# Optimization experiments

Measured on AMD Instinct MI355X. Metric: run time of the kernel, lower is better.

## Reference

```python
import jax, jax.numpy as jnp
import numpy as np

B = 8          # batches
NSX = 8        # subdomains per axis
NSY = 8
NSUB = NSX * NSY
GRID = 64      # points per axis per batch -> 64 points per subdomain
N = B * GRID * GRID
HID = 32       # hidden_channels (also v channels)
OUT = 32       # out_channels
TRES = 64      # max points per subdomain (exact here: uniform grid)


def _point_proj(coords, w1, b1, w2, b2, out_ch, in_ch):
    # PointProjection: Linear(2,hid) -> GELU(exact) -> Linear(hid, out*in) -> [P,out,in]
    h = jax.nn.gelu(coords @ w1 + b1, approximate=False)
    k = h @ w2 + b2
    return k.reshape(coords.shape[0], out_ch, in_ch)


def setup_inputs() -> dict:
    key = jax.random.key(0)
    ks = jax.random.split(key, 9)
    # uniform cell-centered point grid per batch in [0,1]^2
    lin = (jnp.arange(GRID, dtype=jnp.float32) + 0.5) / GRID
    X, Y = jnp.meshgrid(lin, lin, indexing='xy')
    coords1 = jnp.stack([X, Y], axis=-1).reshape(-1, 2)
    src_coords = jnp.tile(coords1, (B, 1))                       # [N,2]
    src_batch = jnp.repeat(jnp.arange(B, dtype=jnp.int32), GRID * GRID)
    v = jax.random.normal(ks[0], (N, HID), jnp.float32)

    def lin_w(k, fan_in, shape):
        bound = 1.0 / np.sqrt(fan_in)
        return jax.random.uniform(k, shape, jnp.float32, -bound, bound)

    return {
        'v': v,
        'src_coords': src_coords,
        'src_batch': src_batch,
        'tgt_res': TRES,
        'src_w1': lin_w(ks[1], 2, (2, HID)),
        'src_b1': lin_w(ks[2], 2, (HID,)),
        'src_w2': lin_w(ks[3], HID, (HID, OUT * HID)),
        'src_b2': lin_w(ks[4], HID, (OUT * HID,)),
        'tgt_w1': lin_w(ks[5], 2, (2, HID)),
        'tgt_b1': lin_w(ks[6], 2, (HID,)),
        'tgt_w2': lin_w(ks[7], HID, (HID, OUT * HID)),
        'tgt_b2': lin_w(ks[8], HID, (OUT * HID,)),
    }


def reference(v, src_coords, src_batch, tgt_res,
              src_w1, src_b1, src_w2, src_b2,
              tgt_w1, tgt_b1, tgt_w2, tgt_b2):
    # --- compute_clusters: assign each point to (batch, subdomain) segment ---
    cx = jnp.clip((src_coords[:, 0] * NSX).astype(jnp.int32), 0, NSX - 1)
    cy = jnp.clip((src_coords[:, 1] * NSY).astype(jnp.int32), 0, NSY - 1)
    seg = src_batch * NSUB + cy * NSX + cx                      # [N]
    S = B * NSUB

    # --- reference target grid in [-1/nsx, 1/nsx] x [-1/nsy, 1/nsy] ---
    x = jnp.linspace(-1.0 / NSX, 1.0 / NSX, tgt_res)
    y = jnp.linspace(-1.0 / NSY, 1.0 / NSY, tgt_res)
    TX, TY = jnp.meshgrid(x, y, indexing='xy')
    tgt_coords = jnp.stack([TX, TY], axis=-1).reshape(-1, 2)    # [T,2], T=tgt_res^2

    # --- per-point MLP kernel projections ---
    psi = _point_proj(src_coords, src_w1, src_b1, src_w2, src_b2, OUT, HID)  # [N,OUT,HID]
    phi = _point_proj(tgt_coords, tgt_w1, tgt_b1, tgt_w2, tgt_b2, OUT, HID)  # [T,OUT,HID]

    # --- segment-wise integral: A[s,o,h] = mean_{x in seg s} psi[x,o,h]*v[x,h] ---
    contrib = psi * v[:, None, :]                                # [N,OUT,HID]
    A = jax.ops.segment_sum(contrib, seg, num_segments=S)        # [S,OUT,HID]
    cnt = jax.ops.segment_sum(jnp.ones((v.shape[0],), v.dtype), seg, num_segments=S)
    A = A / jnp.maximum(cnt, 1.0)[:, None, None]

    # --- contract with target kernel on the reference grid ---
    u = jnp.einsum('toh,soh->sto', phi, A)                       # [S,T,OUT]
    u = u.reshape(B, NSUB, tgt_res, tgt_res, OUT)
    return u
```

## Files before the change

### kernel.cpp

```cpp
#include <hip/hip_runtime.h>
#include <hip/hip_bf16.h>

#define HID   32
#define OUT   32
#define T_TOT 4096
#define S_TOT 512

typedef __attribute__((ext_vector_type(8))) short short8;
typedef __attribute__((ext_vector_type(4))) float f32x4;

__device__ __forceinline__ float gelu_exact(float x) {
    return 0.5f * x * (1.0f + erff(x * 0.70710678118654752440f));
}

__device__ __forceinline__ unsigned int f2bf_u(float x) {
    __hip_bfloat16 h = __float2bfloat16(x);
    unsigned short us = *reinterpret_cast<unsigned short*>(&h);
    return (unsigned int)us;
}

__global__ __launch_bounds__(256) void k_seg_G(
    const float* __restrict__ v, const float* __restrict__ coords,
    const float* __restrict__ sw1, const float* __restrict__ sb1,
    const float* __restrict__ sw2, const float* __restrict__ sb2,
    const float* __restrict__ tw2, const float* __restrict__ tb2,
    const float* __restrict__ tw1, const float* __restrict__ tb1,
    unsigned short* __restrict__ Pbf, float* __restrict__ qout,
    unsigned int* __restrict__ Gbf) {
    const int tid = threadIdx.x;

    if (blockIdx.x >= S_TOT) {
        int t = (blockIdx.x - S_TOT) * 256 + tid;
        int i = t >> 6, j = t & 63;
        const double step = 0.25 / 63.0;
        float x = (float)(-0.125 + (double)j * step);
        float y = (float)(-0.125 + (double)i * step);
        unsigned int pk[16];
#pragma unroll
        for (int c2 = 0; c2 < 16; ++c2) {
            float z0 = fmaf(x, tw1[2 * c2],     fmaf(y, tw1[HID + 2 * c2],     tb1[2 * c2]));
            float z1 = fmaf(x, tw1[2 * c2 + 1], fmaf(y, tw1[HID + 2 * c2 + 1], tb1[2 * c2 + 1]));
            pk[c2] = f2bf_u(gelu_exact(z0)) | (f2bf_u(gelu_exact(z1)) << 16);
        }
        uint4* dst = (uint4*)(Gbf + (size_t)t * 16);
#pragma unroll
        for (int k = 0; k < 4; ++k)
            dst[k] = make_uint4(pk[4 * k], pk[4 * k + 1], pk[4 * k + 2], pk[4 * k + 3]);
        return;
    }

    const int s = blockIdx.x;
    const int b = s >> 6, cy = (s >> 3) & 7, cx = s & 7;

    __shared__ float Hs[64][HID];
    __shared__ float Vs[64][HID];
    __shared__ float Ms[HID][HID];
    __shared__ float Vsum[HID];

    {
        int r = tid >> 2, qq = tid & 3;
        int p = b * 4096 + (cy * 8 + (r >> 3)) * 64 + cx * 8 + (r & 7);
        const f32x4* src = (const f32x4*)(v + (size_t)p * HID + qq * 8);
        f32x4 a0 = src[0], a1 = src[1];
        *(f32x4*)&Vs[r][qq * 8]     = a0;
        *(f32x4*)&Vs[r][qq * 8 + 4] = a1;

        float x = coords[2 * p], y = coords[2 * p + 1];
#pragma unroll
        for (int e = 0; e < 8; ++e) {
            int c = qq * 8 + e;
            float z = fmaf(x, sw1[c], fmaf(y, sw1[HID + c], sb1[c]));
            Hs[r][c] = gelu_exact(z);
        }
    }
    __syncthreads();

    if (tid < 128) {
        int cp = tid >> 3, hq = tid & 7;
        int c0 = cp * 2;
        f32x4 accA = {0.f, 0.f, 0.f, 0.f};
        f32x4 accB = {0.f, 0.f, 0.f, 0.f};
#pragma unroll 16
        for (int r = 0; r < 64; ++r) {
            float2 hv = *(const float2*)&Hs[r][c0];
            f32x4 vv = *(const f32x4*)&Vs[r][hq * 4];
            accA[0] = fmaf(hv.x, vv[0], accA[0]);
            accA[1] = fmaf(hv.x, vv[1], accA[1]);
            accA[2] = fmaf(hv.x, vv[2], accA[2]);
            accA[3] = fmaf(hv.x, vv[3], accA[3]);
            accB[0] = fmaf(hv.y, vv[0], accB[0]);
            accB[1] = fmaf(hv.y, vv[1], accB[1]);
            accB[2] = fmaf(hv.y, vv[2], accB[2]);
            accB[3] = fmaf(hv.y, vv[3], accB[3]);
        }
        *(f32x4*)&Ms[c0][hq * 4]     = accA;
        *(f32x4*)&Ms[c0 + 1][hq * 4] = accB;
    } else if (tid < 160) {
        int h = tid - 128;
        float sum = 0.f;
#pragma unroll 16
        for (int r = 0; r < 64; ++r) sum += Vs[r][h];
        Vsum[h] = sum;
    }
    __syncthreads();

    {
        int o = tid >> 3, hq = tid & 7;
        f32x4 acc = {0.f, 0.f, 0.f, 0.f};
#pragma unroll 8
        for (int c = 0; c < HID; ++c) {
            f32x4 w = *(const f32x4*)(sw2 + (size_t)c * 1024 + o * 32 + hq * 4);
            f32x4 m = *(const f32x4*)&Ms[c][hq * 4];
            acc[0] = fmaf(m[0], w[0], acc[0]);
            acc[1] = fmaf(m[1], w[1], acc[1]);
            acc[2] = fmaf(m[2], w[2], acc[2]);
            acc[3] = fmaf(m[3], w[3], acc[3]);
        }
        f32x4 bb = *(const f32x4*)(sb2 + o * 32 + hq * 4);
        f32x4 vs = *(const f32x4*)&Vsum[hq * 4];
        acc[0] = fmaf(bb[0], vs[0], acc[0]);
        acc[1] = fmaf(bb[1], vs[1], acc[1]);
        acc[2] = fmaf(bb[2], vs[2], acc[2]);
        acc[3] = fmaf(bb[3], vs[3], acc[3]);
        const float inv = 1.0f / 64.0f;
        acc[0] *= inv; acc[1] *= inv; acc[2] *= inv; acc[3] *= inv;

        f32x4 a[8];
        int base = (o & 7) * 8;
#pragma unroll
        for (int k = 0; k < 8; ++k) {
            a[k][0] = __shfl(acc[0], base + k, 64);
            a[k][1] = __shfl(acc[1], base + k, 64);
            a[k][2] = __shfl(acc[2], base + k, 64);
            a[k][3] = __shfl(acc[3], base + k, 64);
        }

        int cq = hq;
        unsigned int pk[2];
#pragma unroll
        for (int k2 = 0; k2 < 2; ++k2) {
            unsigned int w01 = 0;
#pragma unroll
            for (int kk = 0; kk < 2; ++kk) {
                int c = cq * 4 + k2 * 2 + kk;
                float pacc = 0.f;
#pragma unroll
                for (int h8 = 0; h8 < 8; ++h8) {
                    f32x4 w = *(const f32x4*)(tw2 + (size_t)c * 1024 + o * 32 + h8 * 4);
                    pacc = fmaf(w[0], a[h8][0], pacc);
                    pacc = fmaf(w[1], a[h8][1], pacc);
                    pacc = fmaf(w[2], a[h8][2], pacc);
                    pacc = fmaf(w[3], a[h8][3], pacc);
                }
                w01 |= f2bf_u(pacc) << (16 * kk);
            }
            pk[k2] = w01;
        }
        uint2 val; val.x = pk[0]; val.y = pk[1];
        *(uint2*)(Pbf + (size_t)s * 1024 + o * 32 + cq * 4) = val;

        if (cq == 0) {
            float qacc = 0.f;
#pragma unroll
            for (int h8 = 0; h8 < 8; ++h8) {
                f32x4 tb = *(const f32x4*)(tb2 + o * 32 + h8 * 4);
                qacc = fmaf(tb[0], a[h8][0], qacc);
                qacc = fmaf(tb[1], a[h8][1], qacc);
                qacc = fmaf(tb[2], a[h8][2], qacc);
                qacc = fmaf(tb[3], a[h8][3], qacc);
            }
            qout[s * 32 + o] = qacc;
        }
    }
}

__global__ __launch_bounds__(256) void k_contract(
    const unsigned short* __restrict__ Gbf,
    const unsigned short* __restrict__ Pbf,
    const float* __restrict__ q,
    float* __restrict__ u) {
    const int s    = blockIdx.y;
    const int lane = threadIdx.x & 63;
    const int wave = threadIdx.x >> 6;
    const int lo = lane & 15;
    const int lk = lane >> 4;

    const unsigned short* pb = Pbf + (size_t)s * 1024;
    short8 p0 = *(const short8*)(pb + lo * 32 + lk * 8);
    short8 p1 = *(const short8*)(pb + (16 + lo) * 32 + lk * 8);

    f32x4 c0, c1;
#pragma unroll
    for (int j = 0; j < 4; ++j) {
        c0[j] = q[s * 32 + lk * 4 + j];
        c1[j] = q[s * 32 + 16 + lk * 4 + j];
    }

    const int tbase = blockIdx.x * 1024 + wave * 256;
    float* ubase = u + (size_t)s * (T_TOT * 32);

#pragma unroll 4
    for (int tile = 0; tile < 16; ++tile) {
        int t0 = tbase + tile * 16;
        short8 gfrag = *(const short8*)(Gbf + (size_t)(t0 + lo) * 32 + lk * 8);
        f32x4 d0 = __builtin_amdgcn_mfma_f32_16x16x32_bf16(p0, gfrag, c0, 0, 0, 0);
        f32x4 d1 = __builtin_amdgcn_mfma_f32_16x16x32_bf16(p1, gfrag, c1, 0, 0, 0);
        float* up = ubase + (size_t)(t0 + lo) * 32;
        *(f32x4*)(up + lk * 4)      = d0;
        *(f32x4*)(up + 16 + lk * 4) = d1;
    }
}

extern "C" void kernel_launch(void* const* d_in, const int* in_sizes, int n_in,
                              void* d_out, int out_size, void* d_ws, size_t ws_size,
                              hipStream_t stream) {
    (void)in_sizes; (void)n_in; (void)out_size; (void)ws_size;
    const float* v       = (const float*)d_in[0];
    const float* scoords = (const float*)d_in[1];
    const float* sw1 = (const float*)d_in[4];
    const float* sb1 = (const float*)d_in[5];
    const float* sw2 = (const float*)d_in[6];
    const float* sb2 = (const float*)d_in[7];
    const float* tw1 = (const float*)d_in[8];
    const float* tb1 = (const float*)d_in[9];
    const float* tw2 = (const float*)d_in[10];
    const float* tb2 = (const float*)d_in[11];
    float* u = (float*)d_out;

    char* ws = (char*)d_ws;
    unsigned int*   Gbf  = (unsigned int*)ws;
    unsigned short* Pbf  = (unsigned short*)(ws + 262144);
    float*          qbuf = (float*)(ws + 262144 + 1048576);

    hipLaunchKernelGGL(k_seg_G, dim3(S_TOT + 16), dim3(256), 0, stream,
                       v, scoords, sw1, sb1, sw2, sb2, tw2, tb2, tw1, tb1,
                       Pbf, qbuf, Gbf);
    hipLaunchKernelGGL(k_contract, dim3(4, S_TOT), dim3(256), 0, stream,
                       (const unsigned short*)Gbf, (const unsigned short*)Pbf, qbuf, u);
}
```

Before: 64.77 us.

## Fuse segment reduction and contraction into one kernel, hoist target hidden layer

The target-grid hidden-layer computation moves into its own small kernel. The per-segment reduction and the MFMA contraction are fused into a single kernel with one block per segment, and each wave now covers 1024 target points instead of 256. This drops the handoff of P and q through global memory between two large launches and one launch boundary. In exchange, the output write phase falls from 2048 blocks to 512, each doing four times the work. Pbf and q are written and then re-read by the same block after a block-level fence and barrier.

```diff
diff --git a/kernel.cpp b/kernel.cpp
--- a/kernel.cpp
+++ b/kernel.cpp
@@ -19,38 +19,39 @@
     return (unsigned int)us;
 }
 
-__global__ __launch_bounds__(256) void k_seg_G(
+__global__ __launch_bounds__(256) void k_tgt_hidden(
+    const float* __restrict__ tw1, const float* __restrict__ tb1,
+    unsigned int* __restrict__ Gbf ) {
+    int t = blockIdx.x * 256 + threadIdx.x;
+    if (t >= T_TOT) return;
+    int i = t >> 6, j = t & 63;
+    const double step = 0.25 / 63.0;
+    float x = (float)(-0.125 + (double)j * step);
+    float y = (float)(-0.125 + (double)i * step);
+    unsigned int pk[16];
+#pragma unroll
+    for (int c2 = 0; c2 < 16; ++c2) {
+        float z0 = fmaf(x, tw1[2 * c2],     fmaf(y, tw1[HID + 2 * c2],     tb1[2 * c2]));
+        float z1 = fmaf(x, tw1[2 * c2 + 1], fmaf(y, tw1[HID + 2 * c2 + 1], tb1[2 * c2 + 1]));
+        pk[c2] = f2bf_u(gelu_exact(z0)) | (f2bf_u(gelu_exact(z1)) << 16);
+    }
+    uint4* dst = (uint4*)(Gbf + (size_t)t * 16);
+#pragma unroll
+    for (int k = 0; k < 4; ++k)
+        dst[k] = make_uint4(pk[4 * k], pk[4 * k + 1], pk[4 * k + 2], pk[4 * k + 3]);
+}
+
+__global__ __launch_bounds__(256) void k_all(
     const float* __restrict__ v, const float* __restrict__ coords,
     const float* __restrict__ sw1, const float* __restrict__ sb1,
     const float* __restrict__ sw2, const float* __restrict__ sb2,
     const float* __restrict__ tw2, const float* __restrict__ tb2,
-    const float* __restrict__ tw1, const float* __restrict__ tb1,
+    const unsigned short* __restrict__ Gbf,
     unsigned short* __restrict__ Pbf, float* __restrict__ qout,
-    unsigned int* __restrict__ Gbf) {
-    const int tid = threadIdx.x;
-
-    if (blockIdx.x >= S_TOT) {
-        int t = (blockIdx.x - S_TOT) * 256 + tid;
-        int i = t >> 6, j = t & 63;
-        const double step = 0.25 / 63.0;
-        float x = (float)(-0.125 + (double)j * step);
-        float y = (float)(-0.125 + (double)i * step);
-        unsigned int pk[16];
-#pragma unroll
-        for (int c2 = 0; c2 < 16; ++c2) {
-            float z0 = fmaf(x, tw1[2 * c2],     fmaf(y, tw1[HID + 2 * c2],     tb1[2 * c2]));
-            float z1 = fmaf(x, tw1[2 * c2 + 1], fmaf(y, tw1[HID + 2 * c2 + 1], tb1[2 * c2 + 1]));
-            pk[c2] = f2bf_u(gelu_exact(z0)) | (f2bf_u(gelu_exact(z1)) << 16);
-        }
-        uint4* dst = (uint4*)(Gbf + (size_t)t * 16);
-#pragma unroll
-        for (int k = 0; k < 4; ++k)
-            dst[k] = make_uint4(pk[4 * k], pk[4 * k + 1], pk[4 * k + 2], pk[4 * k + 3]);
-        return;
-    }
-
+    float* __restrict__ u) {
     const int s = blockIdx.x;
     const int b = s >> 6, cy = (s >> 3) & 7, cx = s & 7;
+    const int tid = threadIdx.x;
 
     __shared__ float Hs[64][HID];
     __shared__ float Vs[64][HID];
@@ -172,16 +173,12 @@
             qout[s * 32 + o] = qacc;
         }
     }
-}
-
-__global__ __launch_bounds__(256) void k_contract(
-    const unsigned short* __restrict__ Gbf,
-    const unsigned short* __restrict__ Pbf,
-    const float* __restrict__ q,
-    float* __restrict__ u) {
-    const int s    = blockIdx.y;
-    const int lane = threadIdx.x & 63;
-    const int wave = threadIdx.x >> 6;
+
+    __threadfence_block();
+    __syncthreads();
+
+    const int lane = tid & 63;
+    const int wave = tid >> 6;
     const int lo = lane & 15;
     const int lk = lane >> 4;
 
@@ -192,15 +189,15 @@
     f32x4 c0, c1;
 #pragma unroll
     for (int j = 0; j < 4; ++j) {
-        c0[j] = q[s * 32 + lk * 4 + j];
-        c1[j] = q[s * 32 + 16 + lk * 4 + j];
-    }
-
-    const int tbase = blockIdx.x * 1024 + wave * 256;
+        c0[j] = qout[s * 32 + lk * 4 + j];
+        c1[j] = qout[s * 32 + 16 + lk * 4 + j];
+    }
+
+    const int tbase = wave * 1024;
     float* ubase = u + (size_t)s * (T_TOT * 32);
 
 #pragma unroll 4
-    for (int tile = 0; tile < 16; ++tile) {
+    for (int tile = 0; tile < 64; ++tile) {
         int t0 = tbase + tile * 16;
         short8 gfrag = *(const short8*)(Gbf + (size_t)(t0 + lo) * 32 + lk * 8);
         f32x4 d0 = __builtin_amdgcn_mfma_f32_16x16x32_bf16(p0, gfrag, c0, 0, 0, 0);
@@ -232,9 +229,8 @@
     unsigned short* Pbf  = (unsigned short*)(ws + 262144);
     float*          qbuf = (float*)(ws + 262144 + 1048576);
 
-    hipLaunchKernelGGL(k_seg_G, dim3(S_TOT + 16), dim3(256), 0, stream,
-                       v, scoords, sw1, sb1, sw2, sb2, tw2, tb2, tw1, tb1,
-                       Pbf, qbuf, Gbf);
-    hipLaunchKernelGGL(k_contract, dim3(4, S_TOT), dim3(256), 0, stream,
-                       (const unsigned short*)Gbf, (const unsigned short*)Pbf, qbuf, u);
-}
+    hipLaunchKernelGGL(k_tgt_hidden, dim3(16), dim3(256), 0, stream, tw1, tb1, Gbf);
+    hipLaunchKernelGGL(k_all, dim3(S_TOT), dim3(256), 0, stream,
+                       v, scoords, sw1, sb1, sw2, sb2, tw2, tb2,
+                       (const unsigned short*)Gbf, Pbf, qbuf, u);
+}
```

Measured after the change: 72.12 us. 1.11x slower.
